# Performance work log

Measured on AMD Instinct MI355X. Metric: run time of the kernel, lower is better.

## Reference

```python
import jax, jax.numpy as jnp
import numpy as np

B, P, N, M = 8, 50, 128, 128          # batch, pomo, query nodes, route tokens
EMB, H, D = 128, 8, 16                # embedding_dim, head_num, qkv_dim
NE, K = 8, 2                          # num_experts, top-k
CLIP = 10.0                           # logit_clipping


def setup_inputs() -> dict:
    key = jax.random.key(0)
    ks = jax.random.split(key, 12)
    s = 0.02
    return {
        "encoded_nodes": jax.random.normal(ks[0], (B, P, N, EMB), jnp.float32),
        "encoded_routes": jax.random.normal(ks[1], (B, P, M, EMB + 1), jnp.float32),
        "ninf_mask": jnp.zeros((B, P, N), jnp.float32),
        "route_mask": jnp.zeros((B, P, N, M), jnp.float32),
        "Wq": s * jax.random.normal(ks[2], (EMB, H * D), jnp.float32),
        "Wk": s * jax.random.normal(ks[3], (EMB + 1, H * D), jnp.float32),
        "Wv": s * jax.random.normal(ks[4], (EMB + 1, H * D), jnp.float32),
        "Wg": s * jax.random.normal(ks[5], (H * D, NE), jnp.float32),
        "We": s * jax.random.normal(ks[6], (NE, H * D, EMB + 1), jnp.float32),
        "be": jnp.zeros((NE, EMB + 1), jnp.float32),
        "Wfinal": s * jax.random.normal(ks[7], (EMB + 1, 1), jnp.float32),
    }


def _heads(x, W):
    # x: [B,P,n,F] @ W[F,H*D] -> [B,P,H,n,D]
    y = x @ W
    b, p, n, _ = y.shape
    return jnp.swapaxes(y.reshape(b, p, n, H, D), 2, 3)


def reference(encoded_nodes, encoded_routes, ninf_mask, route_mask,
              Wq, Wk, Wv, Wg, We, be, Wfinal):
    # --- masked multi-head attention (multi_head_attention1) ---
    q = _heads(encoded_nodes, Wq)          # [B,P,H,N,D]
    k = _heads(encoded_routes, Wk)         # [B,P,H,M,D]
    v = _heads(encoded_routes, Wv)         # [B,P,H,M,D]
    score = jnp.einsum('bphnd,bphmd->bphnm', q, k) / jnp.sqrt(jnp.float32(D))
    score = score + route_mask[:, :, None, :, :]          # rank3 ninf mask
    w = jax.nn.softmax(score, axis=-1)
    # rank2 mask applied multiplicatively after softmax
    keep = jnp.where(ninf_mask == 0.0, 1.0, 0.0)[:, :, None, :, None]
    w = w * keep
    out = jnp.einsum('bphnm,bphmd->bphnd', w, v)
    out_concat = jnp.swapaxes(out, 2, 3).reshape(B, P, N, H * D)

    # --- top-k gated MoE combine (noisy gating, eval: no noise) ---
    x = out_concat.reshape(-1, H * D)                     # [T, H*D]
    T = x.shape[0]
    gate_logits = x @ Wg                                  # [T, NE]
    top_vals, top_idx = jax.lax.top_k(gate_logits, K)
    top_g = jax.nn.softmax(top_vals, axis=-1)
    gates = jnp.zeros((T, NE), x.dtype).at[jnp.arange(T)[:, None], top_idx].set(top_g)
    expert_out = jnp.einsum('ti,eio->teo', x, We) + be    # [T, NE, EMB+1]
    moe_out = jnp.einsum('te,teo->to', gates, expert_out)
    importance = gates.sum(0)
    moe_loss = importance.var() / (importance.mean() ** 2 + 1e-10)
    mh_atten_out = moe_out.reshape(B, P, N, EMB + 1)

    # --- final scoring ---
    score_scaled = (mh_atten_out @ Wfinal)[..., 0]        # [B,P,N]
    score_clipped = CLIP * jnp.tanh(score_scaled)
    score_masked = score_clipped + ninf_mask
    probs = jax.nn.softmax(score_masked, axis=2)
    return probs, moe_loss
```

## Files before the change

kernel.cpp:

```cpp
#include <hip/hip_runtime.h>

constexpr int B  = 8,  P = 50, N = 128, M = 128;
constexpr int EMB = 128, H = 8, D = 16;
constexpr int NE = 8;
constexpr int HD = H * D;
constexpr int E1 = EMB + 1;
constexpr int BP = B * P;
constexpr int T  = BP * N;

__global__ void prep_kernel(const float* __restrict__ We,
                            const float* __restrict__ be,
                            const float* __restrict__ Wf,
                            float* __restrict__ Wep, float* __restrict__ bpv,
                            float* __restrict__ importance) {
    const int e = blockIdx.x;
    const int f = threadIdx.x;

    float a = 0.f;
    const long base = ((long)e * HD + f) * E1;
    for (int o = 0; o < E1; ++o) a += We[base + o] * Wf[o];
    Wep[e * HD + f] = a;

    if (f == 0) {
        float b = 0.f;
        for (int o = 0; o < E1; ++o) b += be[(long)e * E1 + o] * Wf[o];
        bpv[e] = b;
    }
    if (e == 0 && f < NE) importance[f] = 0.f;
}

__global__ __launch_bounds__(128) void proj_kernel(
    const float* __restrict__ nodes,
    const float* __restrict__ routes,
    const float* __restrict__ Wq, const float* __restrict__ Wk,
    const float* __restrict__ Wv,
    float* __restrict__ qo, float* __restrict__ ko, float* __restrict__ vo) {
    const int mat = blockIdx.y;
    const float* __restrict__ X = (mat == 0) ? nodes : routes;
    const float* __restrict__ W = (mat == 0) ? Wq : (mat == 1 ? Wk : Wv);
    float* __restrict__ out     = (mat == 0) ? qo : (mat == 1 ? ko : vo);
    const int Kd = (mat == 0) ? EMB : E1;

    const int row0 = blockIdx.x * 64;
    const int tid  = threadIdx.x;
    const int tr   = tid >> 4;
    const int tc   = tid & 15;

    __shared__ float XT[8][68];
    __shared__ float WS[8][132];

    float acc[8][8];
    #pragma unroll
    for (int i = 0; i < 8; ++i)
        #pragma unroll
        for (int j = 0; j < 8; ++j) acc[i][j] = 0.f;

    for (int kk = 0; kk < Kd; kk += 8) {
        const int kw = (Kd - kk) < 8 ? (Kd - kk) : 8;
        #pragma unroll
        for (int i = 0; i < 4; ++i) {
            int e = tid + i * 128;
            int kx = e & 7, r = e >> 3;
            XT[kx][r] = (kx < kw) ? X[(long)(row0 + r) * Kd + kk + kx] : 0.f;
        }
        #pragma unroll
        for (int i = 0; i < 2; ++i) {
            int e  = tid + i * 128;
            int kx = e >> 5, c4 = (e & 31) * 4;
            float4 w4 = make_float4(0.f, 0.f, 0.f, 0.f);
            if (kx < kw) w4 = *(const float4*)&W[(long)(kk + kx) * HD + c4];
            *(float4*)&WS[kx][c4] = w4;
        }
        __syncthreads();

        #pragma unroll
        for (int k = 0; k < 8; ++k) {
            float4 xa = *(const float4*)&XT[k][tr * 4];
            float4 xb = *(const float4*)&XT[k][32 + tr * 4];
            float4 wa = *(const float4*)&WS[k][tc * 4];
            float4 wb = *(const float4*)&WS[k][64 + tc * 4];
            float xr[8] = {xa.x, xa.y, xa.z, xa.w, xb.x, xb.y, xb.z, xb.w};
            float wc[8] = {wa.x, wa.y, wa.z, wa.w, wb.x, wb.y, wb.z, wb.w};
            #pragma unroll
            for (int i = 0; i < 8; ++i)
                #pragma unroll
                for (int j = 0; j < 8; ++j) acc[i][j] += xr[i] * wc[j];
        }
        __syncthreads();
    }

    #pragma unroll
    for (int ig = 0; ig < 2; ++ig)
        #pragma unroll
        for (int i = 0; i < 4; ++i) {
            int r = row0 + ig * 32 + tr * 4 + i;
            float4 o0 = make_float4(acc[ig*4+i][0], acc[ig*4+i][1],
                                    acc[ig*4+i][2], acc[ig*4+i][3]);
            float4 o1 = make_float4(acc[ig*4+i][4], acc[ig*4+i][5],
                                    acc[ig*4+i][6], acc[ig*4+i][7]);
            *(float4*)&out[(long)r * HD + tc * 4]      = o0;
            *(float4*)&out[(long)r * HD + 64 + tc * 4] = o1;
        }
}

__global__ __launch_bounds__(64) void attn_kernel(
    const float* __restrict__ qbuf,
    const float* __restrict__ kbuf,
    const float* __restrict__ vbuf,
    const float* __restrict__ rmask,
    const float* __restrict__ ninf,
    float* __restrict__ xcat) {
    const int bp  = blockIdx.x;
    const int h   = blockIdx.y;
    const int tid = threadIdx.x;

    const long t0 = (long)bp * N + tid, t1 = t0 + 64;

    float qr0[16], qr1[16];
    {
        const float4* q0 = (const float4*)&qbuf[t0 * HD + h * D];
        const float4* q1 = (const float4*)&qbuf[t1 * HD + h * D];
        #pragma unroll
        for (int i = 0; i < 4; ++i) {
            float4 a = q0[i], b = q1[i];
            qr0[i*4+0] = a.x*0.25f; qr0[i*4+1] = a.y*0.25f;
            qr0[i*4+2] = a.z*0.25f; qr0[i*4+3] = a.w*0.25f;
            qr1[i*4+0] = b.x*0.25f; qr1[i*4+1] = b.y*0.25f;
            qr1[i*4+2] = b.z*0.25f; qr1[i*4+3] = b.w*0.25f;
        }
    }

    const float* __restrict__ kbase = kbuf + ((long)bp * M) * HD + h * D;
    const float* __restrict__ vbase = vbuf + ((long)bp * M) * HD + h * D;
    const float4* rm0 = (const float4*)&rmask[t0 * M];
    const float4* rm1 = (const float4*)&rmask[t1 * M];

    float sum0 = 0.f, sum1 = 0.f;
    float o0[16], o1[16];
    #pragma unroll
    for (int d = 0; d < 16; ++d) { o0[d] = 0.f; o1[d] = 0.f; }

    for (int mb = 0; mb < 32; ++mb) {
        float4 r0 = rm0[mb], r1 = rm1[mb];
        float r0v[4] = {r0.x, r0.y, r0.z, r0.w};
        float r1v[4] = {r1.x, r1.y, r1.z, r1.w};
        #pragma unroll
        for (int j = 0; j < 4; ++j) {
            const int m = mb * 4 + j;
            const float4* k4 = (const float4*)&kbase[(long)m * HD];
            const float4* v4 = (const float4*)&vbase[(long)m * HD];
            float s0 = 0.f, s1 = 0.f;
            #pragma unroll
            for (int q4 = 0; q4 < 4; ++q4) {
                float4 kq = k4[q4];
                s0 += qr0[q4*4+0]*kq.x + qr0[q4*4+1]*kq.y
                    + qr0[q4*4+2]*kq.z + qr0[q4*4+3]*kq.w;
                s1 += qr1[q4*4+0]*kq.x + qr1[q4*4+1]*kq.y
                    + qr1[q4*4+2]*kq.z + qr1[q4*4+3]*kq.w;
            }
            float e0 = __expf(s0 + r0v[j]);
            float e1 = __expf(s1 + r1v[j]);
            sum0 += e0; sum1 += e1;
            #pragma unroll
            for (int q4 = 0; q4 < 4; ++q4) {
                float4 vq = v4[q4];
                o0[q4*4+0] += e0*vq.x; o0[q4*4+1] += e0*vq.y;
                o0[q4*4+2] += e0*vq.z; o0[q4*4+3] += e0*vq.w;
                o1[q4*4+0] += e1*vq.x; o1[q4*4+1] += e1*vq.y;
                o1[q4*4+2] += e1*vq.z; o1[q4*4+3] += e1*vq.w;
            }
        }
    }

    const float inv0 = ((ninf[t0] == 0.f) ? 1.f : 0.f) / sum0;
    const float inv1 = ((ninf[t1] == 0.f) ? 1.f : 0.f) / sum1;
    #pragma unroll
    for (int q4 = 0; q4 < 4; ++q4) {
        float4 w0 = make_float4(o0[q4*4+0]*inv0, o0[q4*4+1]*inv0,
                                o0[q4*4+2]*inv0, o0[q4*4+3]*inv0);
        float4 w1 = make_float4(o1[q4*4+0]*inv1, o1[q4*4+1]*inv1,
                                o1[q4*4+2]*inv1, o1[q4*4+3]*inv1);
        *(float4*)&xcat[t0 * HD + h * D + q4 * 4] = w0;
        *(float4*)&xcat[t1 * HD + h * D + q4 * 4] = w1;
    }
}

__global__ __launch_bounds__(128) void moe_final_kernel(
    const float* __restrict__ xcat, const float* __restrict__ Wg,
    const float* __restrict__ ninf, const float* __restrict__ Wep,
    const float* __restrict__ bpv, float* __restrict__ importance,
    float* __restrict__ out) {
    __shared__ float WgS[EMB][NE];
    __shared__ float WeS[NE][132];
    __shared__ float red[N];
    __shared__ float impS[NE];

    const int bp = blockIdx.x;
    const int n  = threadIdx.x;

    #pragma unroll
    for (int i = 0; i < 2; ++i) {
        int e = n + i * 128;
        int r = e >> 1, c4 = (e & 1) * 4;
        *(float4*)&WgS[r][c4] = *(const float4*)&Wg[(long)r * NE + c4];
    }
    #pragma unroll
    for (int i = 0; i < 2; ++i) {
        int idx = n + i * 128;
        int r = idx >> 5, c = (idx & 31) * 4;
        *(float4*)&WeS[r][c] = *(const float4*)&Wep[(long)r * HD + c];
    }
    if (n < NE) impS[n] = 0.f;
    __syncthreads();

    const long t = (long)bp * N + n;
    const float4* row4 = (const float4*)&xcat[t * HD];

    float gl[NE];
    #pragma unroll
    for (int e = 0; e < NE; ++e) gl[e] = 0.f;
    for (int fb = 0; fb < 32; ++fb) {
        float4 xv = row4[fb];
        float x4[4] = {xv.x, xv.y, xv.z, xv.w};
        #pragma unroll
        for (int j = 0; j < 4; ++j)
            #pragma unroll
            for (int e = 0; e < NE; ++e) gl[e] += x4[j] * WgS[fb * 4 + j][e];
    }

    int e0 = 0; float v0 = gl[0];
    #pragma unroll
    for (int e = 1; e < NE; ++e) if (gl[e] > v0) { v0 = gl[e]; e0 = e; }
    int e1 = -1; float v1 = -3.4e38f;
    #pragma unroll
    for (int e = 0; e < NE; ++e) if (e != e0 && gl[e] > v1) { v1 = gl[e]; e1 = e; }
    float ex = __expf(v1 - v0);
    float g0 = 1.f / (1.f + ex);
    float g1 = ex / (1.f + ex);

    atomicAdd(&impS[e0], g0);
    atomicAdd(&impS[e1], g1);

    float s = g0 * bpv[e0] + g1 * bpv[e1];
    for (int fb = 0; fb < 32; ++fb) {
        float4 xv = row4[fb];
        float x4[4] = {xv.x, xv.y, xv.z, xv.w};
        #pragma unroll
        for (int j = 0; j < 4; ++j) {
            int f = fb * 4 + j;
            s += x4[j] * (g0 * WeS[e0][f] + g1 * WeS[e1][f]);
        }
    }
    s = 10.f * tanhf(s) + ninf[t];

    red[n] = s;
    __syncthreads();
    for (int off = 64; off > 0; off >>= 1) {
        if (n < off) red[n] = fmaxf(red[n], red[n + off]);
        __syncthreads();
    }
    float mx = red[0];
    __syncthreads();
    float e = __expf(s - mx);
    red[n] = e;
    __syncthreads();
    for (int off = 64; off > 0; off >>= 1) {
        if (n < off) red[n] += red[n + off];
        __syncthreads();
    }
    float sum = red[0];

    out[t] = e / sum;

    if (n < NE) atomicAdd(&importance[n], impS[n]);
}

__global__ void loss_kernel(const float* __restrict__ importance,
                            float* __restrict__ out) {
    if (threadIdx.x == 0) {
        float mean = 0.f;
        #pragma unroll
        for (int e = 0; e < NE; ++e) mean += importance[e];
        mean *= (1.f / NE);
        float var = 0.f;
        #pragma unroll
        for (int e = 0; e < NE; ++e) {
            float d = importance[e] - mean;
            var += d * d;
        }
        var *= (1.f / NE);
        out[T] = var / (mean * mean + 1e-10f);
    }
}

extern "C" void kernel_launch(void* const* d_in, const int* in_sizes, int n_in,
                              void* d_out, int out_size, void* d_ws, size_t ws_size,
                              hipStream_t stream) {
    const float* nodes  = (const float*)d_in[0];
    const float* routes = (const float*)d_in[1];
    const float* ninf   = (const float*)d_in[2];
    const float* rmask  = (const float*)d_in[3];
    const float* Wq     = (const float*)d_in[4];
    const float* Wk     = (const float*)d_in[5];
    const float* Wv     = (const float*)d_in[6];
    const float* Wg     = (const float*)d_in[7];
    const float* We     = (const float*)d_in[8];
    const float* be     = (const float*)d_in[9];
    const float* Wfin   = (const float*)d_in[10];

    float* ws = (float*)d_ws;
    float* Wep        = ws + 16;
    float* bpv        = ws + 1040;
    float* importance = ws + 1048;
    float* qbuf       = ws + 4096;
    float* kbuf       = qbuf + (long)T * HD;
    float* vbuf       = kbuf + (long)T * HD;
    float* xcat       = vbuf + (long)T * HD;

    float* out = (float*)d_out;

    prep_kernel<<<NE, 128, 0, stream>>>(We, be, Wfin, Wep, bpv, importance);
    proj_kernel<<<dim3(800, 3), 128, 0, stream>>>(nodes, routes, Wq, Wk, Wv,
                                                  qbuf, kbuf, vbuf);
    attn_kernel<<<dim3(BP, H), 64, 0, stream>>>(qbuf, kbuf, vbuf,
                                                rmask, ninf, xcat);
    moe_final_kernel<<<BP, 128, 0, stream>>>(xcat, Wg, ninf, Wep, bpv,
                                             importance, out);
    loss_kernel<<<1, 64, 0, stream>>>(importance, out);
}
```

Before: 307.8 us.

## Double-buffer projection GEMM tiles and stage per-head K/V in LDS

The projection kernel now uses 256-thread blocks covering 128 rows, with double-buffered shared-memory tiles. The next K-slice is prefetched into registers while the current one is computed, which halves the barriers per step and hides global load latency. The attention kernel copies each head's K and V rows (128x16) into shared memory once per block, so the 64 threads no longer reload them from global memory in the inner loop. The cost is more LDS per block and higher register pressure, which may reduce occupancy.

```diff
diff --git a/kernel.cpp b/kernel.cpp
--- a/kernel.cpp
+++ b/kernel.cpp
@@ -29,7 +29,7 @@
     if (e == 0 && f < NE) importance[f] = 0.f;
 }
 
-__global__ __launch_bounds__(128) void proj_kernel(
+__global__ __launch_bounds__(256) void proj_kernel(
     const float* __restrict__ nodes,
     const float* __restrict__ routes,
     const float* __restrict__ Wq, const float* __restrict__ Wk,
@@ -40,14 +40,15 @@
     const float* __restrict__ W = (mat == 0) ? Wq : (mat == 1 ? Wk : Wv);
     float* __restrict__ out     = (mat == 0) ? qo : (mat == 1 ? ko : vo);
     const int Kd = (mat == 0) ? EMB : E1;
-
-    const int row0 = blockIdx.x * 64;
+    const int nit = (Kd + 7) >> 3;
+
+    const int row0 = blockIdx.x * 128;
     const int tid  = threadIdx.x;
     const int tr   = tid >> 4;
     const int tc   = tid & 15;
 
-    __shared__ float XT[8][68];
-    __shared__ float WS[8][132];
+    __shared__ float XT[2][8][132];
+    __shared__ float WS[2][8][132];
 
     float acc[8][8];
     #pragma unroll
@@ -55,52 +56,70 @@
         #pragma unroll
         for (int j = 0; j < 8; ++j) acc[i][j] = 0.f;
 
-    for (int kk = 0; kk < Kd; kk += 8) {
-        const int kw = (Kd - kk) < 8 ? (Kd - kk) : 8;
+    float xr[4];
+    float4 wr;
+    const int xkx = tid & 7, xrr = tid >> 3;
+    const int wkx = tid >> 5, wc4 = (tid & 31) * 4;
+
+    {
         #pragma unroll
         for (int i = 0; i < 4; ++i) {
-            int e = tid + i * 128;
-            int kx = e & 7, r = e >> 3;
-            XT[kx][r] = (kx < kw) ? X[(long)(row0 + r) * Kd + kk + kx] : 0.f;
-        }
-        #pragma unroll
-        for (int i = 0; i < 2; ++i) {
-            int e  = tid + i * 128;
-            int kx = e >> 5, c4 = (e & 31) * 4;
-            float4 w4 = make_float4(0.f, 0.f, 0.f, 0.f);
-            if (kx < kw) w4 = *(const float4*)&W[(long)(kk + kx) * HD + c4];
-            *(float4*)&WS[kx][c4] = w4;
-        }
-        __syncthreads();
+            int kg = xkx;
+            xr[i] = (kg < Kd) ? X[(long)(row0 + xrr + i * 32) * Kd + kg] : 0.f;
+        }
+        wr = (wkx < Kd) ? *(const float4*)&W[(long)wkx * HD + wc4]
+                        : make_float4(0.f, 0.f, 0.f, 0.f);
+        #pragma unroll
+        for (int i = 0; i < 4; ++i) XT[0][xkx][xrr + i * 32] = xr[i];
+        *(float4*)&WS[0][wkx][wc4] = wr;
+    }
+    __syncthreads();
+
+    for (int it = 0; it < nit; ++it) {
+        const int buf = it & 1;
+        if (it + 1 < nit) {
+            const int kk = (it + 1) * 8;
+            #pragma unroll
+            for (int i = 0; i < 4; ++i) {
+                int kg = kk + xkx;
+                xr[i] = (kg < Kd) ? X[(long)(row0 + xrr + i * 32) * Kd + kg] : 0.f;
+            }
+            int kg = kk + wkx;
+            wr = (kg < Kd) ? *(const float4*)&W[(long)kg * HD + wc4]
+                           : make_float4(0.f, 0.f, 0.f, 0.f);
+        }
 
         #pragma unroll
         for (int k = 0; k < 8; ++k) {
-            float4 xa = *(const float4*)&XT[k][tr * 4];
-            float4 xb = *(const float4*)&XT[k][32 + tr * 4];
-            float4 wa = *(const float4*)&WS[k][tc * 4];
-            float4 wb = *(const float4*)&WS[k][64 + tc * 4];
-            float xr[8] = {xa.x, xa.y, xa.z, xa.w, xb.x, xb.y, xb.z, xb.w};
-            float wc[8] = {wa.x, wa.y, wa.z, wa.w, wb.x, wb.y, wb.z, wb.w};
+            float4 xa = *(const float4*)&XT[buf][k][tr * 4];
+            float4 xb = *(const float4*)&XT[buf][k][64 + tr * 4];
+            float4 wa = *(const float4*)&WS[buf][k][tc * 4];
+            float4 wb = *(const float4*)&WS[buf][k][64 + tc * 4];
+            float xv[8] = {xa.x, xa.y, xa.z, xa.w, xb.x, xb.y, xb.z, xb.w};
+            float wv[8] = {wa.x, wa.y, wa.z, wa.w, wb.x, wb.y, wb.z, wb.w};
             #pragma unroll
             for (int i = 0; i < 8; ++i)
                 #pragma unroll
-                for (int j = 0; j < 8; ++j) acc[i][j] += xr[i] * wc[j];
+                for (int j = 0; j < 8; ++j) acc[i][j] += xv[i] * wv[j];
+        }
+
+        if (it + 1 < nit) {
+            const int nb = buf ^ 1;
+            #pragma unroll
+            for (int i = 0; i < 4; ++i) XT[nb][xkx][xrr + i * 32] = xr[i];
+            *(float4*)&WS[nb][wkx][wc4] = wr;
         }
         __syncthreads();
     }
 
     #pragma unroll
-    for (int ig = 0; ig < 2; ++ig)
-        #pragma unroll
-        for (int i = 0; i < 4; ++i) {
-            int r = row0 + ig * 32 + tr * 4 + i;
-            float4 o0 = make_float4(acc[ig*4+i][0], acc[ig*4+i][1],
-                                    acc[ig*4+i][2], acc[ig*4+i][3]);
-            float4 o1 = make_float4(acc[ig*4+i][4], acc[ig*4+i][5],
-                                    acc[ig*4+i][6], acc[ig*4+i][7]);
-            *(float4*)&out[(long)r * HD + tc * 4]      = o0;
-            *(float4*)&out[(long)r * HD + 64 + tc * 4] = o1;
-        }
+    for (int i = 0; i < 8; ++i) {
+        int r = row0 + (i < 4 ? 0 : 64) + tr * 4 + (i & 3);
+        float4 o0 = make_float4(acc[i][0], acc[i][1], acc[i][2], acc[i][3]);
+        float4 o1 = make_float4(acc[i][4], acc[i][5], acc[i][6], acc[i][7]);
+        *(float4*)&out[(long)r * HD + tc * 4]      = o0;
+        *(float4*)&out[(long)r * HD + 64 + tc * 4] = o1;
+    }
 }
 
 __global__ __launch_bounds__(64) void attn_kernel(
@@ -114,6 +133,18 @@
     const int h   = blockIdx.y;
     const int tid = threadIdx.x;
 
+    __shared__ float kh[M][D];
+    __shared__ float vh[M][D];
+
+    #pragma unroll
+    for (int i = 0; i < 8; ++i) {
+        int e = tid + i * 64;
+        int r = e >> 2, c4 = (e & 3) * 4;
+        *(float4*)&kh[r][c4] = *(const float4*)&kbuf[((long)bp * M + r) * HD + h * D + c4];
+        *(float4*)&vh[r][c4] = *(const float4*)&vbuf[((long)bp * M + r) * HD + h * D + c4];
+    }
+    __syncthreads();
+
     const long t0 = (long)bp * N + tid, t1 = t0 + 64;
 
     float qr0[16], qr1[16];
@@ -130,8 +161,6 @@
         }
     }
 
-    const float* __restrict__ kbase = kbuf + ((long)bp * M) * HD + h * D;
-    const float* __restrict__ vbase = vbuf + ((long)bp * M) * HD + h * D;
     const float4* rm0 = (const float4*)&rmask[t0 * M];
     const float4* rm1 = (const float4*)&rmask[t1 * M];
 
@@ -147,8 +176,8 @@
         #pragma unroll
         for (int j = 0; j < 4; ++j) {
             const int m = mb * 4 + j;
-            const float4* k4 = (const float4*)&kbase[(long)m * HD];
-            const float4* v4 = (const float4*)&vbase[(long)m * HD];
+            const float4* k4 = (const float4*)&kh[m][0];
+            const float4* v4 = (const float4*)&vh[m][0];
             float s0 = 0.f, s1 = 0.f;
             #pragma unroll
             for (int q4 = 0; q4 < 4; ++q4) {
@@ -320,7 +349,7 @@
     float* out = (float*)d_out;
 
     prep_kernel<<<NE, 128, 0, stream>>>(We, be, Wfin, Wep, bpv, importance);
-    proj_kernel<<<dim3(800, 3), 128, 0, stream>>>(nodes, routes, Wq, Wk, Wv,
+    proj_kernel<<<dim3(400, 3), 256, 0, stream>>>(nodes, routes, Wq, Wk, Wv,
                                                   qbuf, kbuf, vbuf);
     attn_kernel<<<dim3(BP, H), 64, 0, stream>>>(qbuf, kbuf, vbuf,
                                                 rmask, ninf, xcat);
```

Measured after the change: 305.3 us. Within noise of the previous version (-0.8%).
